# Kernel tuning notes

Hardware: AMD Instinct MI355X
Metric: run time of the kernel (lower is better)

## Reference

```python
import jax, jax.numpy as jnp
import numpy as np

CHEB_K = 2  # hops per support; stacked terms = 1 + 2*CHEB_K = 5


def setup_inputs() -> dict:
    key = jax.random.key(0)
    k1, k2, k3, k4, k5 = jax.random.split(key, 5)
    B, N, C, O, D = 16, 1024, 64, 64, 10
    return {
        "x": jax.random.normal(k1, (B, N, C), dtype=jnp.float32),
        "adj": jax.random.uniform(k2, (2, B, N, N), dtype=jnp.float32),
        "node_embedding": jax.random.normal(k3, (N, D), dtype=jnp.float32),
        "weights_pool": jax.random.normal(k4, (D, 2 * CHEB_K + 1, C, O), dtype=jnp.float32) * 0.1,
        "bias_pool": jax.random.normal(k5, (D, O), dtype=jnp.float32) * 0.1,
    }


def reference(x, adj, node_embedding, weights_pool, bias_pool):
    # k-hop graph aggregation over each of the 2 supports
    out = [x]
    for s in range(adj.shape[0]):
        a = adj[s]  # [B, N, N]
        x1 = x
        for _ in range(CHEB_K):
            x1 = jnp.einsum('bnm,bmc->bnc', a, x1)
            out.append(x1)
    x_g = jnp.stack(out, axis=2)  # [B, N, K, C] with K = 2*cheb_k+1 (already node-major)
    # per-node hypernetwork weights and bias from node embeddings
    weights = jnp.einsum('nd,dkio->nkio', node_embedding, weights_pool)  # [N, K, C, O]
    bias = node_embedding @ bias_pool  # [N, O]
    # per-node contraction over (K, C)
    return jnp.einsum('bnki,nkio->bno', x_g, weights) + bias
```

## Files before the change

kernel.cpp:

```cpp
#include <hip/hip_runtime.h>
#include <stdint.h>


typedef __attribute__((ext_vector_type(4))) float f32x4;
typedef __attribute__((ext_vector_type(2))) float f32x2;
typedef __attribute__((ext_vector_type(8))) short s16x8;
typedef __attribute__((ext_vector_type(8))) __bf16 bf16x8;

__device__ __forceinline__ unsigned short f2bf(float f) {
  union { float f; uint32_t u; } v; v.f = f;
  uint32_t r = v.u + 0x7FFFu + ((v.u >> 16) & 1u);
  return (unsigned short)(r >> 16);
}
__device__ __forceinline__ uint32_t pack2(float a, float b) {
  return (uint32_t)f2bf(a) | ((uint32_t)f2bf(b) << 16);
}

union FragU { s16x8 s; bf16x8 b; };

__device__ __forceinline__ void async_cp16(const void* g, void* l) {
  __builtin_amdgcn_global_load_lds(
      (const __attribute__((address_space(1))) void*)g,
      (__attribute__((address_space(3))) void*)l, 16, 0, 0);
}

__global__ __launch_bounds__(256) void cvt_adj(const float* __restrict__ adj,
                                               unsigned short* __restrict__ adjb) {
  const size_t stride = (size_t)gridDim.x * 256 * 8;
  for (size_t p = ((size_t)blockIdx.x * 256 + threadIdx.x) * 8;
       p < 33554432u; p += stride) {
    f32x4 a = *(const f32x4*)(adj + p);
    f32x4 b = *(const f32x4*)(adj + p + 4);
    union { s16x8 s; uint32_t u[4]; } o;
    o.u[0] = pack2(a[0], a[1]);
    o.u[1] = pack2(a[2], a[3]);
    o.u[2] = pack2(b[0], b[1]);
    o.u[3] = pack2(b[2], b[3]);
    *(s16x8*)(adjb + p) = o.s;
  }
}

__global__ __launch_bounds__(256) void prep(const float* __restrict__ x,
                                            const float* __restrict__ wp,
                                            unsigned short* __restrict__ XT0,
                                            float* __restrict__ wpT) {
  __shared__ __align__(16) char smem[17160];
  const int tid = threadIdx.x;
  const int bid = blockIdx.x;
  if (bid < 256) {
    unsigned short (*tl)[72] = (unsigned short(*)[72])smem;
    const int b = bid >> 4, n0 = (bid & 15) * 64;
    {
      const int c4 = (tid & 15) * 4;
#pragma unroll
      for (int i = 0; i < 4; ++i) {
        const int row = (tid >> 4) + i * 16;
        f32x4 v =
            *(const f32x4*)(x + ((size_t)(b * 1024 + n0 + row)) * 64 + c4);
        *(uint32_t*)&tl[row][c4]     = pack2(v[0], v[1]);
        *(uint32_t*)&tl[row][c4 + 2] = pack2(v[2], v[3]);
      }
    }
    __syncthreads();
    {
      const int c = tid >> 2;
      const int nch = (tid & 3) * 16;
      s16x8 s0, s1;
#pragma unroll
      for (int j = 0; j < 8; ++j) {
        s0[j] = (short)tl[nch + j][c];
        s1[j] = (short)tl[nch + 8 + j][c];
      }
      unsigned short* p = XT0 + (size_t)(b * 64 + c) * 1024 + n0 + nch;
      *(s16x8*)p = s0;
      *(s16x8*)(p + 8) = s1;
    }
  } else {
    float (*tl)[65] = (float(*)[65])smem;
    const int jj = bid - 256;
    const int d = jj / 5, ki0 = (jj % 5) * 64;
    const float* src = wp + (size_t)d * 20480;
    {
      const int o4 = (tid & 15) * 4;
#pragma unroll
      for (int i = 0; i < 4; ++i) {
        const int row = (tid >> 4) + i * 16;
        f32x4 v = *(const f32x4*)(src + (size_t)(ki0 + row) * 64 + o4);
        tl[row][o4] = v[0]; tl[row][o4 + 1] = v[1];
        tl[row][o4 + 2] = v[2]; tl[row][o4 + 3] = v[3];
      }
    }
    __syncthreads();
    {
      const int o = tid >> 2;
      const int kch = (tid & 3) * 16;
      float* dst = wpT + (size_t)d * 20480 + (size_t)o * 320 + ki0 + kch;
#pragma unroll
      for (int u = 0; u < 4; ++u) {
        f32x4 v = { tl[kch + 4 * u][o], tl[kch + 4 * u + 1][o],
                    tl[kch + 4 * u + 2][o], tl[kch + 4 * u + 3][o] };
        *(f32x4*)(dst + 4 * u) = v;
      }
    }
  }
}

__device__ __forceinline__ void hop_body(
    char* smem, const unsigned short* __restrict__ A,
    const unsigned short* __restrict__ XT, float* __restrict__ Xout,
    unsigned short* __restrict__ XTout, int write_xt, int rowbase) {
  const int tid = threadIdx.x;
  const int wave = tid >> 6, lane = tid & 63;
  const int l15 = lane & 15, q = lane >> 4;

  unsigned short* const Ast = (unsigned short*)smem;
  unsigned short* const Bst = (unsigned short*)smem + 8192;

  const int sub = lane >> 3;
  const int ch = lane & 7;
  const unsigned short* asrc[2];
  const unsigned short* bsrc[2];
  int ldso[2];
#pragma unroll
  for (int i = 0; i < 2; ++i) {
    const int r = wave * 16 + i * 8 + sub;
    asrc[i] = A + (size_t)(rowbase + r) * 1024 + (ch ^ (r & 7)) * 8;
    bsrc[i] = XT + (size_t)r * 1024 + (ch ^ (r & 7)) * 8;
    ldso[i] = (wave * 16 + i * 8) * 64;
  }

  f32x4 acc[4];
#pragma unroll
  for (int t = 0; t < 4; ++t) acc[t] = (f32x4){0.f, 0.f, 0.f, 0.f};

  auto issue = [&](int s, int k0) {
#pragma unroll
    for (int i = 0; i < 2; ++i) {
      async_cp16(asrc[i] + k0, Ast + s * 4096 + ldso[i]);
      async_cp16(bsrc[i] + k0, Bst + s * 4096 + ldso[i]);
    }
  };
  const int sw = l15 & 7;
  auto compute = [&](int s) {
    const unsigned short* Ab = Ast + s * 4096 + (wave * 16 + l15) * 64;
    const unsigned short* Bb = Bst + s * 4096 + l15 * 64;
#pragma unroll
    for (int h = 0; h < 2; ++h) {
      const int cko = ((h * 4 + q) ^ sw) * 8;
      FragU af;
      af.s = *(const s16x8*)(Ab + cko);
#pragma unroll
      for (int t = 0; t < 4; ++t) {
        FragU bf;
        bf.s = *(const s16x8*)(Bb + t * 1024 + cko);
        acc[t] = __builtin_amdgcn_mfma_f32_16x16x32_bf16(af.b, bf.b, acc[t],
                                                         0, 0, 0);
      }
    }
  };

  issue(0, 0);
#pragma unroll 1
  for (int kt = 0; kt < 16; ++kt) {
    const int cur = kt & 1;
    __syncthreads();
    if (kt + 1 < 16) issue(cur ^ 1, (kt + 1) * 64);
    compute(cur);
  }

  __syncthreads();
  float (*tile)[65] = (float(*)[65])smem;
#pragma unroll
  for (int t = 0; t < 4; ++t)
#pragma unroll
    for (int rr = 0; rr < 4; ++rr)
      tile[wave * 16 + q * 4 + rr][t * 16 + l15] = acc[t][rr];
  __syncthreads();

  {
    const int row = tid >> 2;
    const int cb = (tid & 3) * 16;
    float* __restrict__ outp = Xout + (size_t)(rowbase + row) * 64 + cb;
#pragma unroll
    for (int u = 0; u < 4; ++u) {
      f32x4 v = { tile[row][cb + 4 * u], tile[row][cb + 4 * u + 1],
                  tile[row][cb + 4 * u + 2], tile[row][cb + 4 * u + 3] };
      *(f32x4*)(outp + 4 * u) = v;
    }
  }
  if (write_xt) {
    const int c = tid >> 2;
    const int nch = (tid & 3) * 16;
    unsigned short* __restrict__ xtp = XTout + (size_t)c * 1024 + rowbase + nch;
    s16x8 s0, s1;
#pragma unroll
    for (int j = 0; j < 8; ++j) {
      s0[j] = (short)f2bf(tile[nch + j][c]);
      s1[j] = (short)f2bf(tile[nch + 8 + j][c]);
    }
    *(s16x8*)xtp = s0;
    *(s16x8*)(xtp + 8) = s1;
  }
}

__global__ __launch_bounds__(256, 4) void hop1_kernel(
    const unsigned short* __restrict__ adjb,
    const unsigned short* __restrict__ XT0, float* __restrict__ X1,
    unsigned short* __restrict__ XT1, const float* __restrict__ wpT,
    const float* __restrict__ emb, unsigned short* __restrict__ WT) {
  __shared__ __align__(16) char smem[32768];
  const int bx = blockIdx.x, slice = blockIdx.y, b = slice & 15;
  hop_body(smem, adjb + (size_t)slice * 1048576, XT0 + (size_t)b * 65536,
           X1 + (size_t)slice * 65536, XT1 + (size_t)slice * 65536, 1,
           bx * 64);

  const int bid = slice * 16 + bx;
  const int tid = threadIdx.x;
#pragma unroll 1
  for (int j = bid * 5; j < bid * 5 + 5; ++j) {
    const int jx = j % 40;
    const int n0 = (j / 40) * 16;
    const int idx = (jx * 256 + tid) * 2;
    f32x2 wv[10];
#pragma unroll
    for (int d = 0; d < 10; ++d)
      wv[d] = *(const f32x2*)(wpT + (size_t)d * 20480 + idx);
#pragma unroll
    for (int g = 0; g < 16; ++g) {
      float a0 = 0.f, a1 = 0.f;
#pragma unroll
      for (int d = 0; d < 10; ++d) {
        const float e = emb[(n0 + g) * 10 + d];
        a0 += e * wv[d][0];
        a1 += e * wv[d][1];
      }
      *(uint32_t*)(WT + (size_t)(n0 + g) * 20480 + idx) = pack2(a0, a1);
    }
  }
}

__global__ __launch_bounds__(256, 4) void hop2_kernel(
    const unsigned short* __restrict__ adjb,
    const unsigned short* __restrict__ XT1, float* __restrict__ X2) {
  __shared__ __align__(16) char smem[32768];
  const int bx = 15 - (int)blockIdx.x;
  const int slice = 31 - (int)blockIdx.y;
  hop_body(smem, adjb + (size_t)slice * 1048576, XT1 + (size_t)slice * 65536,
           X2 + (size_t)slice * 65536, (unsigned short*)0, 0, bx * 64);
}

__global__ __launch_bounds__(256, 2) void final_kernel(
    const float* __restrict__ x, const float* __restrict__ X1,
    const float* __restrict__ X2, const unsigned short* __restrict__ WT,
    const float* __restrict__ emb, const float* __restrict__ bias_pool,
    float* __restrict__ out) {
  __shared__ unsigned short xg[2][16][328];
  const int tid = threadIdx.x;
  const int node_base = blockIdx.x * 2;

  for (int u = tid; u < 5120; u += 256) {
    const int nd = u / 2560;
    int rem = u - nd * 2560;
    const int bb = rem / 160;
    const int kiu = rem - bb * 160;
    const int ki = kiu * 2;
    const int k = ki >> 6;
    const int c = ki & 63;
    const int nn = node_base + nd;
    const float* src;
    if (k == 0) {
      src = x + ((size_t)bb * 1024 + nn) * 64 + c;
    } else {
      const float* arr = (k == 1 || k == 3) ? X1 : X2;
      const int s = (k >= 3) ? 1 : 0;
      src = arr + ((size_t)(s * 16 + bb) * 1024 + nn) * 64 + c;
    }
    f32x2 v = *(const f32x2*)src;
    *(uint32_t*)&xg[nd][bb][ki] = pack2(v[0], v[1]);
  }
  __syncthreads();

  const int wave = tid >> 6, lane = tid & 63;
  const int nd = wave >> 1, oh = wave & 1;
  const int l15 = lane & 15, q = lane >> 4;
  const int n = node_base + nd;
  f32x4 acc[2];
#pragma unroll
  for (int t = 0; t < 2; ++t) acc[t] = (f32x4){0.f, 0.f, 0.f, 0.f};

  const unsigned short* wt0 =
      WT + (size_t)n * 20480 + (size_t)l15 * 320 + q * 8;
#pragma unroll
  for (int ks = 0; ks < 10; ++ks) {
    const int k0 = ks * 32;
    FragU af;
    af.s = *(const s16x8*)&xg[nd][l15][k0 + q * 8];
#pragma unroll
    for (int tt = 0; tt < 2; ++tt) {
      const int t = oh * 2 + tt;
      FragU bf;
      bf.s = *(const s16x8*)(wt0 + (size_t)t * (16 * 320) + k0);
      acc[tt] = __builtin_amdgcn_mfma_f32_16x16x32_bf16(af.b, bf.b, acc[tt],
                                                        0, 0, 0);
    }
  }

#pragma unroll
  for (int tt = 0; tt < 2; ++tt) {
    const int o = (oh * 2 + tt) * 16 + l15;
    float bv = 0.f;
#pragma unroll
    for (int d = 0; d < 10; ++d)
      bv += emb[n * 10 + d] * bias_pool[d * 64 + o];
#pragma unroll
    for (int rr = 0; rr < 4; ++rr) {
      const int bb = q * 4 + rr;
      out[((size_t)bb * 1024 + n) * 64 + o] = acc[tt][rr] + bv;
    }
  }
}

extern "C" void kernel_launch(void* const* d_in, const int* in_sizes, int n_in,
                              void* d_out, int out_size, void* d_ws,
                              size_t ws_size, hipStream_t stream) {
  const float* x   = (const float*)d_in[0];
  const float* adj = (const float*)d_in[1];
  const float* emb = (const float*)d_in[2];
  const float* wp  = (const float*)d_in[3];
  const float* bp  = (const float*)d_in[4];
  float* out = (float*)d_out;

  char* ws = (char*)d_ws;
  unsigned short* XT0 = (unsigned short*)(ws);
  unsigned short* XT1 = (unsigned short*)(ws + ((size_t)2 << 20));
  float* X1  = (float*)(ws + ((size_t)6 << 20));
  float* X2  = (float*)(ws + ((size_t)14 << 20));
  float* wpT = (float*)(ws + ((size_t)22 << 20));
  unsigned short* WT = (unsigned short*)(ws + ((size_t)23 << 20));
  unsigned short* adjb = (unsigned short*)(ws + ((size_t)64 << 20));

  cvt_adj<<<dim3(8192), dim3(256), 0, stream>>>(adj, adjb);
  prep<<<dim3(306), dim3(256), 0, stream>>>(x, wp, XT0, wpT);
  hop1_kernel<<<dim3(16, 32), dim3(256), 0, stream>>>(adjb, XT0, X1, XT1,
                                                      wpT, emb, WT);
  hop2_kernel<<<dim3(16, 32), dim3(256), 0, stream>>>(adjb, XT1, X2);
  final_kernel<<<dim3(512), dim3(256), 0, stream>>>(x, X1, X2, WT, emb, bp,
                                                    out);
}
```

Baseline: 270.7 us.

## Drop adjacency bf16 pre-pass, convert fp32 tiles in-kernel, factor hypernetwork weights

Removes the separate adj fp32->bf16 conversion kernel and has each hop kernel stream fp32 adjacency tiles into LDS, packing them to bf16 in registers before the MFMA. The per-node weight materialisation (WT, about 40MB of bf16) is removed: the final kernel contracts against each of the 10 pool slices of bf16 weights and combines them with the embedding scalars. Hop outputs X1/X2 are stored as bf16 to halve intermediate traffic. The cost is twice the adjacency bytes read per hop (fp32 read twice instead of one conversion pass plus two bf16 reads), higher LDS use that lowers occupancy to 3 blocks per SM, and ten times more MFMA work in the final kernel.

```diff
diff --git a/kernel.cpp b/kernel.cpp
--- a/kernel.cpp
+++ b/kernel.cpp
@@ -16,7 +16,7 @@
   return (uint32_t)f2bf(a) | ((uint32_t)f2bf(b) << 16);
 }
 
-union FragU { s16x8 s; bf16x8 b; };
+union FragU { s16x8 s; bf16x8 b; uint32_t u[4]; };
 
 __device__ __forceinline__ void async_cp16(const void* g, void* l) {
   __builtin_amdgcn_global_load_lds(
@@ -24,26 +24,10 @@
       (__attribute__((address_space(3))) void*)l, 16, 0, 0);
 }
 
-__global__ __launch_bounds__(256) void cvt_adj(const float* __restrict__ adj,
-                                               unsigned short* __restrict__ adjb) {
-  const size_t stride = (size_t)gridDim.x * 256 * 8;
-  for (size_t p = ((size_t)blockIdx.x * 256 + threadIdx.x) * 8;
-       p < 33554432u; p += stride) {
-    f32x4 a = *(const f32x4*)(adj + p);
-    f32x4 b = *(const f32x4*)(adj + p + 4);
-    union { s16x8 s; uint32_t u[4]; } o;
-    o.u[0] = pack2(a[0], a[1]);
-    o.u[1] = pack2(a[2], a[3]);
-    o.u[2] = pack2(b[0], b[1]);
-    o.u[3] = pack2(b[2], b[3]);
-    *(s16x8*)(adjb + p) = o.s;
-  }
-}
-
 __global__ __launch_bounds__(256) void prep(const float* __restrict__ x,
                                             const float* __restrict__ wp,
                                             unsigned short* __restrict__ XT0,
-                                            float* __restrict__ wpT) {
+                                            unsigned short* __restrict__ wpTb) {
   __shared__ __align__(16) char smem[17160];
   const int tid = threadIdx.x;
   const int bid = blockIdx.x;
@@ -94,39 +78,47 @@
     {
       const int o = tid >> 2;
       const int kch = (tid & 3) * 16;
-      float* dst = wpT + (size_t)d * 20480 + (size_t)o * 320 + ki0 + kch;
-#pragma unroll
-      for (int u = 0; u < 4; ++u) {
-        f32x4 v = { tl[kch + 4 * u][o], tl[kch + 4 * u + 1][o],
-                    tl[kch + 4 * u + 2][o], tl[kch + 4 * u + 3][o] };
-        *(f32x4*)(dst + 4 * u) = v;
-      }
+      unsigned short* dst =
+          wpTb + (size_t)d * 20480 + (size_t)o * 320 + ki0 + kch;
+      s16x8 s0, s1;
+#pragma unroll
+      for (int j = 0; j < 8; ++j) {
+        s0[j] = (short)f2bf(tl[kch + j][o]);
+        s1[j] = (short)f2bf(tl[kch + 8 + j][o]);
+      }
+      *(s16x8*)dst = s0;
+      *(s16x8*)(dst + 8) = s1;
     }
   }
 }
 
 __device__ __forceinline__ void hop_body(
-    char* smem, const unsigned short* __restrict__ A,
-    const unsigned short* __restrict__ XT, float* __restrict__ Xout,
+    char* smem, const float* __restrict__ A,
+    const unsigned short* __restrict__ XT, unsigned short* __restrict__ Xoutb,
     unsigned short* __restrict__ XTout, int write_xt, int rowbase) {
   const int tid = threadIdx.x;
   const int wave = tid >> 6, lane = tid & 63;
   const int l15 = lane & 15, q = lane >> 4;
 
-  unsigned short* const Ast = (unsigned short*)smem;
-  unsigned short* const Bst = (unsigned short*)smem + 8192;
-
-  const int sub = lane >> 3;
-  const int ch = lane & 7;
-  const unsigned short* asrc[2];
+  float* const Ast = (float*)smem;
+  unsigned short* const Bst = (unsigned short*)(smem + 32768);
+
+  const float* asrc[4];
+  int aldso[4];
+#pragma unroll
+  for (int i = 0; i < 4; ++i) {
+    const int r = wave * 16 + i * 4 + (lane >> 4);
+    const int gch = (lane & 15) ^ (r & 7);
+    asrc[i] = A + (size_t)(rowbase + r) * 1024 + gch * 4;
+    aldso[i] = (wave * 16 + i * 4) * 64;
+  }
   const unsigned short* bsrc[2];
-  int ldso[2];
+  int bldso[2];
 #pragma unroll
   for (int i = 0; i < 2; ++i) {
-    const int r = wave * 16 + i * 8 + sub;
-    asrc[i] = A + (size_t)(rowbase + r) * 1024 + (ch ^ (r & 7)) * 8;
-    bsrc[i] = XT + (size_t)r * 1024 + (ch ^ (r & 7)) * 8;
-    ldso[i] = (wave * 16 + i * 8) * 64;
+    const int r = wave * 16 + i * 8 + (lane >> 3);
+    bsrc[i] = XT + (size_t)r * 1024 + ((lane & 7) ^ (r & 7)) * 8;
+    bldso[i] = (wave * 16 + i * 8) * 64;
   }
 
   f32x4 acc[4];
@@ -135,20 +127,27 @@
 
   auto issue = [&](int s, int k0) {
 #pragma unroll
-    for (int i = 0; i < 2; ++i) {
-      async_cp16(asrc[i] + k0, Ast + s * 4096 + ldso[i]);
-      async_cp16(bsrc[i] + k0, Bst + s * 4096 + ldso[i]);
-    }
+    for (int i = 0; i < 4; ++i)
+      async_cp16(asrc[i] + k0, Ast + s * 4096 + aldso[i]);
+#pragma unroll
+    for (int i = 0; i < 2; ++i)
+      async_cp16(bsrc[i] + k0, Bst + s * 4096 + bldso[i]);
   };
   const int sw = l15 & 7;
   auto compute = [&](int s) {
-    const unsigned short* Ab = Ast + s * 4096 + (wave * 16 + l15) * 64;
+    const float* Ab = Ast + s * 4096 + (wave * 16 + l15) * 64;
     const unsigned short* Bb = Bst + s * 4096 + l15 * 64;
 #pragma unroll
     for (int h = 0; h < 2; ++h) {
+      const int g0 = h * 8 + q * 2;
+      f32x4 lo = *(const f32x4*)(Ab + (g0 ^ sw) * 4);
+      f32x4 hi = *(const f32x4*)(Ab + ((g0 + 1) ^ sw) * 4);
+      FragU af;
+      af.u[0] = pack2(lo[0], lo[1]);
+      af.u[1] = pack2(lo[2], lo[3]);
+      af.u[2] = pack2(hi[0], hi[1]);
+      af.u[3] = pack2(hi[2], hi[3]);
       const int cko = ((h * 4 + q) ^ sw) * 8;
-      FragU af;
-      af.s = *(const s16x8*)(Ab + cko);
 #pragma unroll
       for (int t = 0; t < 4; ++t) {
         FragU bf;
@@ -180,13 +179,16 @@
   {
     const int row = tid >> 2;
     const int cb = (tid & 3) * 16;
-    float* __restrict__ outp = Xout + (size_t)(rowbase + row) * 64 + cb;
-#pragma unroll
-    for (int u = 0; u < 4; ++u) {
-      f32x4 v = { tile[row][cb + 4 * u], tile[row][cb + 4 * u + 1],
-                  tile[row][cb + 4 * u + 2], tile[row][cb + 4 * u + 3] };
-      *(f32x4*)(outp + 4 * u) = v;
-    }
+    unsigned short* __restrict__ outp =
+        Xoutb + (size_t)(rowbase + row) * 64 + cb;
+    s16x8 s0, s1;
+#pragma unroll
+    for (int j = 0; j < 8; ++j) {
+      s0[j] = (short)f2bf(tile[row][cb + j]);
+      s1[j] = (short)f2bf(tile[row][cb + 8 + j]);
+    }
+    *(s16x8*)outp = s0;
+    *(s16x8*)(outp + 8) = s1;
   }
   if (write_xt) {
     const int c = tid >> 2;
@@ -203,57 +205,31 @@
   }
 }
 
-__global__ __launch_bounds__(256, 4) void hop1_kernel(
-    const unsigned short* __restrict__ adjb,
-    const unsigned short* __restrict__ XT0, float* __restrict__ X1,
-    unsigned short* __restrict__ XT1, const float* __restrict__ wpT,
-    const float* __restrict__ emb, unsigned short* __restrict__ WT) {
-  __shared__ __align__(16) char smem[32768];
+__global__ __launch_bounds__(256, 3) void hop1_kernel(
+    const float* __restrict__ adj, const unsigned short* __restrict__ XT0,
+    unsigned short* __restrict__ X1b, unsigned short* __restrict__ XT1) {
+  __shared__ __align__(16) char smem[49152];
   const int bx = blockIdx.x, slice = blockIdx.y, b = slice & 15;
-  hop_body(smem, adjb + (size_t)slice * 1048576, XT0 + (size_t)b * 65536,
-           X1 + (size_t)slice * 65536, XT1 + (size_t)slice * 65536, 1,
+  hop_body(smem, adj + (size_t)slice * 1048576, XT0 + (size_t)b * 65536,
+           X1b + (size_t)slice * 65536, XT1 + (size_t)slice * 65536, 1,
            bx * 64);
-
-  const int bid = slice * 16 + bx;
-  const int tid = threadIdx.x;
-#pragma unroll 1
-  for (int j = bid * 5; j < bid * 5 + 5; ++j) {
-    const int jx = j % 40;
-    const int n0 = (j / 40) * 16;
-    const int idx = (jx * 256 + tid) * 2;
-    f32x2 wv[10];
-#pragma unroll
-    for (int d = 0; d < 10; ++d)
-      wv[d] = *(const f32x2*)(wpT + (size_t)d * 20480 + idx);
-#pragma unroll
-    for (int g = 0; g < 16; ++g) {
-      float a0 = 0.f, a1 = 0.f;
-#pragma unroll
-      for (int d = 0; d < 10; ++d) {
-        const float e = emb[(n0 + g) * 10 + d];
-        a0 += e * wv[d][0];
-        a1 += e * wv[d][1];
-      }
-      *(uint32_t*)(WT + (size_t)(n0 + g) * 20480 + idx) = pack2(a0, a1);
-    }
-  }
-}
-
-__global__ __launch_bounds__(256, 4) void hop2_kernel(
-    const unsigned short* __restrict__ adjb,
-    const unsigned short* __restrict__ XT1, float* __restrict__ X2) {
-  __shared__ __align__(16) char smem[32768];
+}
+
+__global__ __launch_bounds__(256, 3) void hop2_kernel(
+    const float* __restrict__ adj, const unsigned short* __restrict__ XT1,
+    unsigned short* __restrict__ X2b) {
+  __shared__ __align__(16) char smem[49152];
   const int bx = 15 - (int)blockIdx.x;
   const int slice = 31 - (int)blockIdx.y;
-  hop_body(smem, adjb + (size_t)slice * 1048576, XT1 + (size_t)slice * 65536,
-           X2 + (size_t)slice * 65536, (unsigned short*)0, 0, bx * 64);
+  hop_body(smem, adj + (size_t)slice * 1048576, XT1 + (size_t)slice * 65536,
+           X2b + (size_t)slice * 65536, (unsigned short*)0, 0, bx * 64);
 }
 
 __global__ __launch_bounds__(256, 2) void final_kernel(
-    const float* __restrict__ x, const float* __restrict__ X1,
-    const float* __restrict__ X2, const unsigned short* __restrict__ WT,
-    const float* __restrict__ emb, const float* __restrict__ bias_pool,
-    float* __restrict__ out) {
+    const float* __restrict__ x, const unsigned short* __restrict__ X1b,
+    const unsigned short* __restrict__ X2b,
+    const unsigned short* __restrict__ wpTb, const float* __restrict__ emb,
+    const float* __restrict__ bias_pool, float* __restrict__ out) {
   __shared__ unsigned short xg[2][16][328];
   const int tid = threadIdx.x;
   const int node_base = blockIdx.x * 2;
@@ -267,16 +243,16 @@
     const int k = ki >> 6;
     const int c = ki & 63;
     const int nn = node_base + nd;
-    const float* src;
+    uint32_t w;
     if (k == 0) {
-      src = x + ((size_t)bb * 1024 + nn) * 64 + c;
+      f32x2 v = *(const f32x2*)(x + ((size_t)bb * 1024 + nn) * 64 + c);
+      w = pack2(v[0], v[1]);
     } else {
-      const float* arr = (k == 1 || k == 3) ? X1 : X2;
+      const unsigned short* arr = (k == 1 || k == 3) ? X1b : X2b;
       const int s = (k >= 3) ? 1 : 0;
-      src = arr + ((size_t)(s * 16 + bb) * 1024 + nn) * 64 + c;
-    }
-    f32x2 v = *(const f32x2*)src;
-    *(uint32_t*)&xg[nd][bb][ki] = pack2(v[0], v[1]);
+      w = *(const uint32_t*)(arr + ((size_t)(s * 16 + bb) * 1024 + nn) * 64 + c);
+    }
+    *(uint32_t*)&xg[nd][bb][ki] = w;
   }
   __syncthreads();
 
@@ -284,25 +260,39 @@
   const int nd = wave >> 1, oh = wave & 1;
   const int l15 = lane & 15, q = lane >> 4;
   const int n = node_base + nd;
+
+  FragU af[10];
+#pragma unroll
+  for (int ks = 0; ks < 10; ++ks)
+    af[ks].s = *(const s16x8*)&xg[nd][l15][ks * 32 + q * 8];
+
   f32x4 acc[2];
-#pragma unroll
-  for (int t = 0; t < 2; ++t) acc[t] = (f32x4){0.f, 0.f, 0.f, 0.f};
-
-  const unsigned short* wt0 =
-      WT + (size_t)n * 20480 + (size_t)l15 * 320 + q * 8;
-#pragma unroll
-  for (int ks = 0; ks < 10; ++ks) {
-    const int k0 = ks * 32;
-    FragU af;
-    af.s = *(const s16x8*)&xg[nd][l15][k0 + q * 8];
-#pragma unroll
-    for (int tt = 0; tt < 2; ++tt) {
-      const int t = oh * 2 + tt;
-      FragU bf;
-      bf.s = *(const s16x8*)(wt0 + (size_t)t * (16 * 320) + k0);
-      acc[tt] = __builtin_amdgcn_mfma_f32_16x16x32_bf16(af.b, bf.b, acc[tt],
-                                                        0, 0, 0);
-    }
+  acc[0] = (f32x4){0.f, 0.f, 0.f, 0.f};
+  acc[1] = (f32x4){0.f, 0.f, 0.f, 0.f};
+
+  const unsigned short* wb0 = wpTb + (size_t)(oh * 32 + l15) * 320 + q * 8;
+#pragma unroll 1
+  for (int d = 0; d < 10; ++d) {
+    const unsigned short* wd = wb0 + (size_t)d * 20480;
+    f32x4 tmp[2];
+    tmp[0] = (f32x4){0.f, 0.f, 0.f, 0.f};
+    tmp[1] = (f32x4){0.f, 0.f, 0.f, 0.f};
+#pragma unroll
+    for (int ks = 0; ks < 10; ++ks) {
+#pragma unroll
+      for (int tt = 0; tt < 2; ++tt) {
+        FragU bf;
+        bf.s = *(const s16x8*)(wd + tt * 5120 + ks * 32);
+        tmp[tt] = __builtin_amdgcn_mfma_f32_16x16x32_bf16(af[ks].b, bf.b,
+                                                          tmp[tt], 0, 0, 0);
+      }
+    }
+    const float e = emb[n * 10 + d];
+#pragma unroll
+    for (int tt = 0; tt < 2; ++tt)
+#pragma unroll
+      for (int rr = 0; rr < 4; ++rr)
+        acc[tt][rr] += e * tmp[tt][rr];
   }
 
 #pragma unroll
@@ -331,19 +321,15 @@
   float* out = (float*)d_out;
 
   char* ws = (char*)d_ws;
-  unsigned short* XT0 = (unsigned short*)(ws);
-  unsigned short* XT1 = (unsigned short*)(ws + ((size_t)2 << 20));
-  float* X1  = (float*)(ws + ((size_t)6 << 20));
-  float* X2  = (float*)(ws + ((size_t)14 << 20));
-  float* wpT = (float*)(ws + ((size_t)22 << 20));
-  unsigned short* WT = (unsigned short*)(ws + ((size_t)23 << 20));
-  unsigned short* adjb = (unsigned short*)(ws + ((size_t)64 << 20));
-
-  cvt_adj<<<dim3(8192), dim3(256), 0, stream>>>(adj, adjb);
-  prep<<<dim3(306), dim3(256), 0, stream>>>(x, wp, XT0, wpT);
-  hop1_kernel<<<dim3(16, 32), dim3(256), 0, stream>>>(adjb, XT0, X1, XT1,
-                                                      wpT, emb, WT);
-  hop2_kernel<<<dim3(16, 32), dim3(256), 0, stream>>>(adjb, XT1, X2);
-  final_kernel<<<dim3(512), dim3(256), 0, stream>>>(x, X1, X2, WT, emb, bp,
-                                                    out);
-}
+  unsigned short* XT0  = (unsigned short*)(ws);
+  unsigned short* XT1  = (unsigned short*)(ws + ((size_t)2 << 20));
+  unsigned short* X1b  = (unsigned short*)(ws + ((size_t)6 << 20));
+  unsigned short* X2b  = (unsigned short*)(ws + ((size_t)10 << 20));
+  unsigned short* wpTb = (unsigned short*)(ws + ((size_t)14 << 20));
+
+  prep<<<dim3(306), dim3(256), 0, stream>>>(x, wp, XT0, wpTb);
+  hop1_kernel<<<dim3(16, 32), dim3(256), 0, stream>>>(adj, XT0, X1b, XT1);
+  hop2_kernel<<<dim3(16, 32), dim3(256), 0, stream>>>(adj, XT1, X2b);
+  final_kernel<<<dim3(512), dim3(256), 0, stream>>>(x, X1b, X2b, wpTb, emb,
+                                                    bp, out);
+}
```

Result: slower. 290.9 us (+7.5%).
